# Kernel optimization log

Measured on AMD Instinct MI355X. Metric: run time of the kernel, lower is better.

Reference implementation:

```python
import jax, jax.numpy as jnp
import numpy as np


def setup_inputs() -> dict:
    key = jax.random.key(0)
    k1, k2 = jax.random.split(key)
    B, L, V, D = 8, 2048, 1024, 1024
    hidden_states = jax.random.normal(k1, (B, L, D), dtype=jnp.float32)
    visual_hidden_state = jax.random.normal(k2, (B, V, D), dtype=jnp.float32)
    return {"hidden_states": hidden_states, "visual_hidden_state": visual_hidden_state}


def reference(hidden_states, visual_hidden_state):
    # fusion_scores = H @ V^T  (no scaling, no masking)
    scores = jnp.einsum("bld,bvd->blv", hidden_states, visual_hidden_state)
    probs = jax.nn.softmax(scores, axis=-1)
    # fusion_output = probs @ V
    return jnp.einsum("blv,bvd->bld", probs, visual_hidden_state)
```

## Files before the change

### kernel.cpp

```cpp
#include <hip/hip_runtime.h>


typedef _Float16 half8_t __attribute__((ext_vector_type(8)));
typedef _Float16 half4_t __attribute__((ext_vector_type(4)));
typedef __fp16   fp16x2  __attribute__((ext_vector_type(2)));
typedef float    f32x4   __attribute__((ext_vector_type(4)));

#define B_ 8
#define L_ 2048
#define V_ 1024
#define D_ 1024

__device__ __forceinline__ half8_t cvt8(f32x4 a, f32x4 b) {
  union { half8_t h; fp16x2 p[4]; } u;
  u.p[0] = __builtin_amdgcn_cvt_pkrtz(a[0], a[1]);
  u.p[1] = __builtin_amdgcn_cvt_pkrtz(a[2], a[3]);
  u.p[2] = __builtin_amdgcn_cvt_pkrtz(b[0], b[1]);
  u.p[3] = __builtin_amdgcn_cvt_pkrtz(b[2], b[3]);
  return u.h;
}
__device__ __forceinline__ half4_t cvt4(f32x4 a) {
  union { half4_t h; fp16x2 p[2]; } u;
  u.p[0] = __builtin_amdgcn_cvt_pkrtz(a[0], a[1]);
  u.p[1] = __builtin_amdgcn_cvt_pkrtz(a[2], a[3]);
  return u.h;
}

__device__ __forceinline__ void gload_lds16(const _Float16* g, _Float16* l) {
  __builtin_amdgcn_global_load_lds(
      (const __attribute__((address_space(1))) unsigned int*)(g),
      (__attribute__((address_space(3))) unsigned int*)(l), 16, 0, 0);
}

__global__ __launch_bounds__(256) void p0_hconv(const float* __restrict__ H,
                                                _Float16* __restrict__ Hh) {
  const size_t i = ((size_t)blockIdx.x * 256 + threadIdx.x) * 8;
  f32x4 a = *(const f32x4*)(H + i);
  f32x4 b = *(const f32x4*)(H + i + 4);
  *(half8_t*)(Hh + i) = cvt8(a, b);
}

__global__ __launch_bounds__(256) void p1_vconv(const float* __restrict__ V,
                                                _Float16* __restrict__ Vh,
                                                _Float16* __restrict__ VTh) {
  const int b  = blockIdx.z;
  const int d0 = blockIdx.x * 64;
  const int v0 = blockIdx.y * 64;
  const float* Vb = V + (size_t)b * V_ * D_;
  __shared__ __align__(16) _Float16 Lt[64 * 80];
  const int t   = threadIdx.x;
  const int dc4 = (t & 15) * 4;
  #pragma unroll
  for (int it = 0; it < 4; ++it) {
    const int vr = (t >> 4) + it * 16;
    f32x4 x = *(const f32x4*)(Vb + (size_t)(v0 + vr) * D_ + d0 + dc4);
    half4_t h = cvt4(x);
    *(half4_t*)(Vh + (size_t)b * V_ * D_ + (size_t)(v0 + vr) * D_ + d0 + dc4) = h;
    #pragma unroll
    for (int j = 0; j < 4; ++j) Lt[(dc4 + j) * 80 + vr] = h[j];
  }
  __syncthreads();
  #pragma unroll
  for (int it = 0; it < 2; ++it) {
    const int dr = (t >> 3) + it * 32;
    const int vc = (t & 7) * 8;
    half8_t y = *(const half8_t*)&Lt[dr * 80 + vc];
    *(half8_t*)(VTh + (size_t)b * D_ * V_ + (size_t)(d0 + dr) * V_ + v0 + vc) = y;
  }
}

#define PH_BAR() asm volatile("s_barrier" ::: "memory")

__global__ __launch_bounds__(512, 2) void gemm256(
    const _Float16* __restrict__ A, const _Float16* __restrict__ B,
    float* __restrict__ C) {
  int lin = blockIdx.x;
  lin = (lin & 7) * 32 + (lin >> 3);
  const int bz = lin >> 5;
  const int my = (lin >> 2) & 7;
  const int nx = lin & 3;
  const int m0 = my * 256, n0 = nx * 256;

  const _Float16* Ap = A + (size_t)bz * (2048 * 1024) + (size_t)m0 * 1024;
  const _Float16* Bp = B + (size_t)bz * (1024 * 1024) + (size_t)n0 * 1024;
  float*          Cp = C + (size_t)bz * (2048 * 1024);

  __shared__ __align__(16) _Float16 As[2][16384];
  __shared__ __align__(16) _Float16 Bs[2][16384];

  const int t    = threadIdx.x;
  const int lane = t & 63;
  const int wid  = t >> 6;
  const int wm   = wid >> 2;
  const int wn   = wid & 3;
  const int fr   = lane & 15;
  const int fk   = lane >> 4;

  f32x4 acc[8][4];
  {
    f32x4 z = {0.f, 0.f, 0.f, 0.f};
    #pragma unroll
    for (int i = 0; i < 8; ++i)
      #pragma unroll
      for (int j = 0; j < 4; ++j) acc[i][j] = z;
  }

  #define STG(PTR, ARR, BUFL, H, KTT)                                          \
    {                                                                          \
      _Pragma("unroll")                                                        \
      for (int i_ = 0; i_ < 2; ++i_) {                                         \
        const int c_ = i_ * 512 + t;                                           \
        const int kg_ = c_ >> 7, r_ = c_ & 127;                                \
        gload_lds16(PTR + (size_t)((H) * 128 + r_) * 1024 + (KTT) * 64 + kg_ * 8, \
                    &ARR[BUFL][(kg_ * 256 + (H) * 128 + r_) * 8]);             \
      }                                                                        \
    }

  #define LDA(BUFL, mt_, ks_) \
    (*(const half8_t*)&As[BUFL][(((ks_) * 4 + fk) * 256 + wm * 128 + (mt_) * 16 + fr) * 8])
  #define LDB(BUFL, nt_, ks_) \
    (*(const half8_t*)&Bs[BUFL][(((ks_) * 4 + fk) * 256 + wn * 64 + (nt_) * 16 + fr) * 8])

  #define MFMA16(AF, BF, MOFF, NOFF)                                           \
    __builtin_amdgcn_s_setprio(1);                                             \
    _Pragma("unroll")                                                          \
    for (int ks = 0; ks < 2; ++ks)                                             \
      _Pragma("unroll")                                                        \
      for (int nt = 0; nt < 2; ++nt)                                           \
        _Pragma("unroll")                                                      \
        for (int mt = 0; mt < 4; ++mt)                                         \
          acc[(MOFF) + mt][(NOFF) + nt] =                                      \
              __builtin_amdgcn_mfma_f32_16x16x32_f16(                          \
                  AF[mt][ks], BF[nt][ks], acc[(MOFF) + mt][(NOFF) + nt], 0, 0, 0); \
    __builtin_amdgcn_s_setprio(0);

  #define TILE(KT, BUFL)                                                       \
    {                                                                          \
      half8_t a[4][2], b0[2][2], b1[2][2];                                     \
                         \
      _Pragma("unroll")                                                        \
      for (int ks = 0; ks < 2; ++ks) {                                         \
        _Pragma("unroll")                                                      \
        for (int mt = 0; mt < 4; ++mt) a[mt][ks] = LDA(BUFL, mt, ks);          \
        _Pragma("unroll")                                                      \
        for (int nt = 0; nt < 2; ++nt) b0[nt][ks] = LDB(BUFL, nt, ks);         \
      }                                                                        \
      PH_BAR();                                                                \
      MFMA16(a, b0, 0, 0)                                                      \
      PH_BAR();                                                                \
                   \
      _Pragma("unroll")                                                        \
      for (int ks = 0; ks < 2; ++ks)                                           \
        _Pragma("unroll")                                                      \
        for (int nt = 0; nt < 2; ++nt) b1[nt][ks] = LDB(BUFL, 2 + nt, ks);     \
      if ((KT) < 14) { STG(Bp, Bs, BUFL, 0, (KT) + 2) }                        \
      PH_BAR();                                                                \
      MFMA16(a, b1, 0, 2)                                                      \
      PH_BAR();                                                                \
                   \
      _Pragma("unroll")                                                        \
      for (int ks = 0; ks < 2; ++ks)                                           \
        _Pragma("unroll")                                                      \
        for (int mt = 0; mt < 4; ++mt) a[mt][ks] = LDA(BUFL, 4 + mt, ks);      \
      if ((KT) < 14) { STG(Bp, Bs, BUFL, 1, (KT) + 2) }                        \
      PH_BAR();                                                                \
      MFMA16(a, b1, 4, 2)                                                      \
      PH_BAR();                                                                \
                \
      if ((KT) < 14) { STG(Ap, As, BUFL, 0, (KT) + 2) STG(Ap, As, BUFL, 1, (KT) + 2) } \
      PH_BAR();                                                                \
      MFMA16(a, b0, 4, 0)                                                      \
      if ((KT) <= 13) {                                                        \
        asm volatile("s_waitcnt vmcnt(8)" ::: "memory");                       \
      } else if ((KT) == 14) {                                                 \
        asm volatile("s_waitcnt vmcnt(0)" ::: "memory");                       \
      }                                                                        \
      PH_BAR();                                                                \
    }

  STG(Bp, Bs, 0, 0, 0) STG(Ap, As, 0, 0, 0) STG(Bp, Bs, 0, 1, 0) STG(Ap, As, 0, 1, 0)
  STG(Bp, Bs, 1, 0, 1) STG(Ap, As, 1, 0, 1) STG(Bp, Bs, 1, 1, 1) STG(Ap, As, 1, 1, 1)
  asm volatile("s_waitcnt vmcnt(8)" ::: "memory");
  PH_BAR();

  #pragma unroll 1
  for (int ktp = 0; ktp < 8; ++ktp) {
    TILE(2 * ktp, 0)
    TILE(2 * ktp + 1, 1)
  }
  #undef TILE
  #undef STG
  #undef LDA
  #undef LDB
  #undef MFMA16

  const int rq = (lane >> 4) * 4;
  const int cb = n0 + wn * 64 + (lane & 15);
  const int rb = m0 + wm * 128 + rq;
  #pragma unroll
  for (int mt = 0; mt < 8; ++mt)
    #pragma unroll
    for (int nt = 0; nt < 4; ++nt) {
      #pragma unroll
      for (int r = 0; r < 4; ++r)
        Cp[(size_t)(rb + mt * 16 + r) * 1024 + cb + nt * 16] = acc[mt][nt][r];
    }
}

__global__ __launch_bounds__(256) void k2_softmax(const float* __restrict__ S,
                                                  _Float16* __restrict__ P) {
  const int t    = threadIdx.x;
  const int lane = t & 63;
  const int row  = blockIdx.x * 4 + (t >> 6);
  const float* Sr = S + (size_t)row * V_;

  f32x4 s[4];
  #pragma unroll
  for (int j = 0; j < 4; ++j) s[j] = *(const f32x4*)(Sr + (lane + 64 * j) * 4);

  float m = -1e30f;
  #pragma unroll
  for (int j = 0; j < 4; ++j)
    m = fmaxf(m, fmaxf(fmaxf(s[j][0], s[j][1]), fmaxf(s[j][2], s[j][3])));
  #pragma unroll
  for (int off = 1; off < 64; off <<= 1) m = fmaxf(m, __shfl_xor(m, off, 64));

  float sum = 0.f;
  #pragma unroll
  for (int j = 0; j < 4; ++j) {
    s[j][0] = __expf(s[j][0] - m); s[j][1] = __expf(s[j][1] - m);
    s[j][2] = __expf(s[j][2] - m); s[j][3] = __expf(s[j][3] - m);
    sum += (s[j][0] + s[j][1]) + (s[j][2] + s[j][3]);
  }
  #pragma unroll
  for (int off = 1; off < 64; off <<= 1) sum += __shfl_xor(sum, off, 64);
  const float inv = 1.0f / sum;

  _Float16* Pr = P + (size_t)row * V_;
  #pragma unroll
  for (int j = 0; j < 4; ++j) {
    f32x4 e = {s[j][0] * inv, s[j][1] * inv, s[j][2] * inv, s[j][3] * inv};
    *(half4_t*)(Pr + (lane + 64 * j) * 4) = cvt4(e);
  }
}

__global__ __launch_bounds__(256, 2) void k1_slow(
    const float* __restrict__ H, const float* __restrict__ Vv, float* __restrict__ S) {
  const int b  = blockIdx.z;
  const int m0 = blockIdx.y * 128;
  const int n0 = blockIdx.x * 128;
  const float* Hb = H  + (size_t)b * L_ * D_;
  const float* Vb = Vv + (size_t)b * V_ * D_;
  float*       Sb = S  + (size_t)b * L_ * V_;
  __shared__ __align__(16) _Float16 As[2][4096];
  __shared__ __align__(16) _Float16 Bs[2][4096];
  const int t = threadIdx.x, lane = t & 63, wm = (t >> 6) >> 1, wn = (t >> 6) & 1;
  f32x4 acc[4][4];
  { f32x4 z = {0,0,0,0};
    #pragma unroll
    for (int i = 0; i < 4; ++i)
      #pragma unroll
      for (int j = 0; j < 4; ++j) acc[i][j] = z; }
  const int skg = t & 3, sm = t >> 2;
  for (int kt = 0; kt < 32; ++kt) {
    const int kbase = kt * 32 + skg * 8, buf = kt & 1;
    #pragma unroll
    for (int h = 0; h < 2; ++h) {
      const int m = sm + h * 64;
      const float* sa = Hb + (size_t)(m0 + m) * D_ + kbase;
      const float* sb = Vb + (size_t)(n0 + m) * D_ + kbase;
      const int cell = skg * 128 + (m ^ (skg * 2));
      *(half8_t*)&As[buf][cell * 8] = cvt8(*(const f32x4*)sa, *(const f32x4*)(sa + 4));
      *(half8_t*)&Bs[buf][cell * 8] = cvt8(*(const f32x4*)sb, *(const f32x4*)(sb + 4));
    }
    __syncthreads();
    const int fkg = lane >> 4, fr = lane & 15;
    half8_t af[4];
    #pragma unroll
    for (int mt = 0; mt < 4; ++mt)
      af[mt] = *(const half8_t*)&As[buf][(fkg * 128 + ((wm * 64 + mt * 16 + fr) ^ (fkg * 2))) * 8];
    #pragma unroll
    for (int nt = 0; nt < 4; ++nt) {
      half8_t bf = *(const half8_t*)&Bs[buf][(fkg * 128 + ((wn * 64 + nt * 16 + fr) ^ (fkg * 2))) * 8];
      #pragma unroll
      for (int mt = 0; mt < 4; ++mt)
        acc[mt][nt] = __builtin_amdgcn_mfma_f32_16x16x32_f16(af[mt], bf, acc[mt][nt], 0, 0, 0);
    }
  }
  const int rq = (lane >> 4) * 4;
  #pragma unroll
  for (int mt = 0; mt < 4; ++mt)
    #pragma unroll
    for (int nt = 0; nt < 4; ++nt) {
      const int col = n0 + wn * 64 + nt * 16 + (lane & 15);
      const int rb  = m0 + wm * 64 + mt * 16 + rq;
      #pragma unroll
      for (int r = 0; r < 4; ++r) Sb[(size_t)(rb + r) * V_ + col] = acc[mt][nt][r];
    }
}

__global__ __launch_bounds__(256) void k2_slow(float* __restrict__ S) {
  const int row = blockIdx.x;
  float* Sr = S + (size_t)row * V_;
  const int t = threadIdx.x;
  f32x4 s = ((const f32x4*)Sr)[t];
  float m = fmaxf(fmaxf(s[0], s[1]), fmaxf(s[2], s[3]));
  #pragma unroll
  for (int off = 1; off < 64; off <<= 1) m = fmaxf(m, __shfl_xor(m, off, 64));
  __shared__ float redm[4];
  __shared__ float reds[4];
  const int w = t >> 6;
  if ((t & 63) == 0) redm[w] = m;
  __syncthreads();
  m = fmaxf(fmaxf(redm[0], redm[1]), fmaxf(redm[2], redm[3]));
  const float e0 = __expf(s[0] - m), e1 = __expf(s[1] - m);
  const float e2 = __expf(s[2] - m), e3 = __expf(s[3] - m);
  float sum = (e0 + e1) + (e2 + e3);
  #pragma unroll
  for (int off = 1; off < 64; off <<= 1) sum += __shfl_xor(sum, off, 64);
  if ((t & 63) == 0) reds[w] = sum;
  __syncthreads();
  const float inv = 1.0f / ((reds[0] + reds[1]) + (reds[2] + reds[3]));
  half4_t p;
  p[0] = (_Float16)(e0 * inv); p[1] = (_Float16)(e1 * inv);
  p[2] = (_Float16)(e2 * inv); p[3] = (_Float16)(e3 * inv);
  *(half4_t*)((_Float16*)Sr + 4 * t) = p;
}

__global__ __launch_bounds__(512, 2) void k3_slow(
    const float* __restrict__ Vv, float* __restrict__ O) {
  const int b = blockIdx.y, r0 = blockIdx.x * 64;
  const float* Vb = Vv + (size_t)b * V_ * D_;
  float*       Ob = O  + (size_t)b * L_ * D_;
  const _Float16* Pb = (const _Float16*)Ob;
  __shared__ __align__(16) _Float16 Bs[32768];
  const int t = threadIdx.x, lane = t & 63, w = t >> 6;
  f32x4 acc[4][8];
  { f32x4 z = {0,0,0,0};
    #pragma unroll
    for (int i = 0; i < 4; ++i)
      #pragma unroll
      for (int j = 0; j < 8; ++j) acc[i][j] = z; }
  for (int kt = 0; kt < 32; ++kt) {
    const int v0 = kt * 32;
    #pragma unroll
    for (int i = 0; i < 8; ++i) {
      const int c = t + i * 512, kg = c >> 10, d = c & 1023;
      const float* src = Vb + (size_t)(v0 + kg * 8) * D_ + d;
      f32x4 x0, x1;
      x0[0] = src[0*D_]; x0[1] = src[1*D_]; x0[2] = src[2*D_]; x0[3] = src[3*D_];
      x1[0] = src[4*D_]; x1[1] = src[5*D_]; x1[2] = src[6*D_]; x1[3] = src[7*D_];
      *(half8_t*)&Bs[(kg * 1024 + d) * 8] = cvt8(x0, x1);
    }
    __syncthreads();
    const int fkg = lane >> 4, fr = lane & 15;
    half8_t af[4];
    #pragma unroll
    for (int mt = 0; mt < 4; ++mt)
      af[mt] = *(const half8_t*)(Pb + (size_t)(r0 + mt * 16 + fr) * 2048 + v0 + fkg * 8);
    #pragma unroll
    for (int nt = 0; nt < 8; ++nt) {
      half8_t bf = *(const half8_t*)&Bs[(fkg * 1024 + w * 128 + nt * 16 + fr) * 8];
      #pragma unroll
      for (int mt = 0; mt < 4; ++mt)
        acc[mt][nt] = __builtin_amdgcn_mfma_f32_16x16x32_f16(af[mt], bf, acc[mt][nt], 0, 0, 0);
    }
    __syncthreads();
  }
  const int rq = (lane >> 4) * 4;
  #pragma unroll
  for (int mt = 0; mt < 4; ++mt)
    #pragma unroll
    for (int nt = 0; nt < 8; ++nt) {
      const int col = w * 128 + nt * 16 + (lane & 15);
      const int rb  = r0 + mt * 16 + rq;
      #pragma unroll
      for (int r = 0; r < 4; ++r) Ob[(size_t)(rb + r) * D_ + col] = acc[mt][nt][r];
    }
}

extern "C" void kernel_launch(void* const* d_in, const int* in_sizes, int n_in,
                              void* d_out, int out_size, void* d_ws, size_t ws_size,
                              hipStream_t stream) {
  (void)in_sizes; (void)n_in; (void)out_size;
  const float* H  = (const float*)d_in[0];
  const float* Vv = (const float*)d_in[1];
  float* O = (float*)d_out;

  const size_t need = (size_t)64 * 1024 * 1024;
  if (ws_size >= need && d_ws != nullptr) {
    _Float16* Hh  = (_Float16*)d_ws;
    _Float16* Vh  = Hh + (size_t)B_ * L_ * D_;
    _Float16* VTh = Vh + (size_t)B_ * V_ * D_;
    _Float16* P   = Hh;

    p0_hconv<<<dim3((B_ * L_ * D_) / (256 * 8)), 256, 0, stream>>>(H, Hh);
    p1_vconv<<<dim3(D_ / 64, V_ / 64, B_), 256, 0, stream>>>(Vv, Vh, VTh);
    gemm256<<<dim3(256), 512, 0, stream>>>(Hh, Vh, O);
    k2_softmax<<<dim3(B_ * L_ / 4), 256, 0, stream>>>(O, P);
    gemm256<<<dim3(256), 512, 0, stream>>>(P, VTh, O);
  } else {
    k1_slow<<<dim3(V_ / 128, L_ / 128, B_), 256, 0, stream>>>(H, Vv, O);
    k2_slow<<<dim3(B_ * L_), 256, 0, stream>>>(O);
    k3_slow<<<dim3(L_ / 64, B_), 512, 0, stream>>>(Vv, O);
  }
}
```

Before: 255.0 us.

## Merge conversion kernels and simplify GEMM pipeline to one-tile-ahead prefetch

Fuses the H and V fp16 conversion kernels into one launch that dispatches on block index, removing one kernel launch. The GEMM main loop drops the fine-grained staggered prefetch, the per-phase barriers and the setprio hints. Instead it issues the whole next tile's global-to-LDS loads at the start of each tile and waits on vmcnt(0) plus a single barrier at the end. This trades deeper, finer-grained overlap for fewer barriers, so memory latency may be less hidden and MFMA issue priority is lost.

```diff
diff --git a/kernel.cpp b/kernel.cpp
--- a/kernel.cpp
+++ b/kernel.cpp
@@ -32,23 +32,25 @@
       (__attribute__((address_space(3))) unsigned int*)(l), 16, 0, 0);
 }
 
-__global__ __launch_bounds__(256) void p0_hconv(const float* __restrict__ H,
-                                                _Float16* __restrict__ Hh) {
-  const size_t i = ((size_t)blockIdx.x * 256 + threadIdx.x) * 8;
-  f32x4 a = *(const f32x4*)(H + i);
-  f32x4 b = *(const f32x4*)(H + i + 4);
-  *(half8_t*)(Hh + i) = cvt8(a, b);
-}
-
-__global__ __launch_bounds__(256) void p1_vconv(const float* __restrict__ V,
+__global__ __launch_bounds__(256) void p01_conv(const float* __restrict__ H,
+                                                _Float16* __restrict__ Hh,
+                                                const float* __restrict__ V,
                                                 _Float16* __restrict__ Vh,
                                                 _Float16* __restrict__ VTh) {
-  const int b  = blockIdx.z;
-  const int d0 = blockIdx.x * 64;
-  const int v0 = blockIdx.y * 64;
+  const int t = threadIdx.x;
+  if (blockIdx.x < 8192) {
+    const size_t i = ((size_t)blockIdx.x * 256 + t) * 8;
+    f32x4 a = *(const f32x4*)(H + i);
+    f32x4 b = *(const f32x4*)(H + i + 4);
+    *(half8_t*)(Hh + i) = cvt8(a, b);
+    return;
+  }
+  const int lin = blockIdx.x - 8192;
+  const int b   = lin >> 8;
+  const int d0  = (lin & 15) * 64;
+  const int v0  = ((lin >> 4) & 15) * 64;
   const float* Vb = V + (size_t)b * V_ * D_;
   __shared__ __align__(16) _Float16 Lt[64 * 80];
-  const int t   = threadIdx.x;
   const int dc4 = (t & 15) * 4;
   #pragma unroll
   for (int it = 0; it < 4; ++it) {
@@ -68,8 +70,6 @@
     *(half8_t*)(VTh + (size_t)b * D_ * V_ + (size_t)(d0 + dr) * V_ + v0 + vc) = y;
   }
 }
-
-#define PH_BAR() asm volatile("s_barrier" ::: "memory")
 
 __global__ __launch_bounds__(512, 2) void gemm256(
     const _Float16* __restrict__ A, const _Float16* __restrict__ B,
@@ -115,6 +115,9 @@
                     &ARR[BUFL][(kg_ * 256 + (H) * 128 + r_) * 8]);             \
       }                                                                        \
     }
+  #define STGTILE(BUFL, KTT) \
+    STG(Bp, Bs, BUFL, 0, KTT) STG(Ap, As, BUFL, 0, KTT) \
+    STG(Bp, Bs, BUFL, 1, KTT) STG(Ap, As, BUFL, 1, KTT)
 
   #define LDA(BUFL, mt_, ks_) \
     (*(const half8_t*)&As[BUFL][(((ks_) * 4 + fk) * 256 + wm * 128 + (mt_) * 16 + fr) * 8])
@@ -122,7 +125,6 @@
     (*(const half8_t*)&Bs[BUFL][(((ks_) * 4 + fk) * 256 + wn * 64 + (nt_) * 16 + fr) * 8])
 
   #define MFMA16(AF, BF, MOFF, NOFF)                                           \
-    __builtin_amdgcn_s_setprio(1);                                             \
     _Pragma("unroll")                                                          \
     for (int ks = 0; ks < 2; ++ks)                                             \
       _Pragma("unroll")                                                        \
@@ -131,13 +133,13 @@
         for (int mt = 0; mt < 4; ++mt)                                         \
           acc[(MOFF) + mt][(NOFF) + nt] =                                      \
               __builtin_amdgcn_mfma_f32_16x16x32_f16(                          \
-                  AF[mt][ks], BF[nt][ks], acc[(MOFF) + mt][(NOFF) + nt], 0, 0, 0); \
-    __builtin_amdgcn_s_setprio(0);
-
-  #define TILE(KT, BUFL)                                                       \
+                  AF[mt][ks], BF[nt][ks], acc[(MOFF) + mt][(NOFF) + nt], 0, 0, 0);
+
+  #define TILE(KT, BUFL, OTH)                                                  \
     {                                                                          \
+      if ((KT) < 15) { STGTILE(OTH, (KT) + 1) }                                \
+      __builtin_amdgcn_sched_barrier(0);            \
       half8_t a[4][2], b0[2][2], b1[2][2];                                     \
-                         \
       _Pragma("unroll")                                                        \
       for (int ks = 0; ks < 2; ++ks) {                                         \
         _Pragma("unroll")                                                      \
@@ -145,65 +147,50 @@
         _Pragma("unroll")                                                      \
         for (int nt = 0; nt < 2; ++nt) b0[nt][ks] = LDB(BUFL, nt, ks);         \
       }                                                                        \
-      PH_BAR();                                                                \
       MFMA16(a, b0, 0, 0)                                                      \
-      PH_BAR();                                                                \
-                   \
       _Pragma("unroll")                                                        \
       for (int ks = 0; ks < 2; ++ks)                                           \
         _Pragma("unroll")                                                      \
         for (int nt = 0; nt < 2; ++nt) b1[nt][ks] = LDB(BUFL, 2 + nt, ks);     \
-      if ((KT) < 14) { STG(Bp, Bs, BUFL, 0, (KT) + 2) }                        \
-      PH_BAR();                                                                \
       MFMA16(a, b1, 0, 2)                                                      \
-      PH_BAR();                                                                \
-                   \
       _Pragma("unroll")                                                        \
       for (int ks = 0; ks < 2; ++ks)                                           \
         _Pragma("unroll")                                                      \
         for (int mt = 0; mt < 4; ++mt) a[mt][ks] = LDA(BUFL, 4 + mt, ks);      \
-      if ((KT) < 14) { STG(Bp, Bs, BUFL, 1, (KT) + 2) }                        \
-      PH_BAR();                                                                \
       MFMA16(a, b1, 4, 2)                                                      \
-      PH_BAR();                                                                \
-                \
-      if ((KT) < 14) { STG(Ap, As, BUFL, 0, (KT) + 2) STG(Ap, As, BUFL, 1, (KT) + 2) } \
-      PH_BAR();                                                                \
       MFMA16(a, b0, 4, 0)                                                      \
-      if ((KT) <= 13) {                                                        \
-        asm volatile("s_waitcnt vmcnt(8)" ::: "memory");                       \
-      } else if ((KT) == 14) {                                                 \
+      if ((KT) < 15) {                                                         \
         asm volatile("s_waitcnt vmcnt(0)" ::: "memory");                       \
+        __builtin_amdgcn_s_barrier();                                          \
       }                                                                        \
-      PH_BAR();                                                                \
-    }
-
-  STG(Bp, Bs, 0, 0, 0) STG(Ap, As, 0, 0, 0) STG(Bp, Bs, 0, 1, 0) STG(Ap, As, 0, 1, 0)
-  STG(Bp, Bs, 1, 0, 1) STG(Ap, As, 1, 0, 1) STG(Bp, Bs, 1, 1, 1) STG(Ap, As, 1, 1, 1)
-  asm volatile("s_waitcnt vmcnt(8)" ::: "memory");
-  PH_BAR();
+    }
+
+  STGTILE(0, 0)
+  asm volatile("s_waitcnt vmcnt(0)" ::: "memory");
+  __builtin_amdgcn_s_barrier();
 
   #pragma unroll 1
-  for (int ktp = 0; ktp < 8; ++ktp) {
-    TILE(2 * ktp, 0)
-    TILE(2 * ktp + 1, 1)
+  for (int tp = 0; tp < 8; ++tp) {
+    TILE(2 * tp, 0, 1)
+    TILE(2 * tp + 1, 1, 0)
   }
   #undef TILE
+  #undef STGTILE
   #undef STG
   #undef LDA
   #undef LDB
   #undef MFMA16
 
   const int rq = (lane >> 4) * 4;
-  const int cb = n0 + wn * 64 + (lane & 15);
-  const int rb = m0 + wm * 128 + rq;
   #pragma unroll
   for (int mt = 0; mt < 8; ++mt)
     #pragma unroll
     for (int nt = 0; nt < 4; ++nt) {
+      const int col   = n0 + wn * 64 + nt * 16 + (lane & 15);
+      const int rbase = m0 + wm * 128 + mt * 16 + rq;
       #pragma unroll
       for (int r = 0; r < 4; ++r)
-        Cp[(size_t)(rb + mt * 16 + r) * 1024 + cb + nt * 16] = acc[mt][nt][r];
+        Cp[(size_t)(rbase + r) * 1024 + col] = acc[mt][nt][r];
     }
 }
 
@@ -394,8 +381,7 @@
     _Float16* VTh = Vh + (size_t)B_ * V_ * D_;
     _Float16* P   = Hh;
 
-    p0_hconv<<<dim3((B_ * L_ * D_) / (256 * 8)), 256, 0, stream>>>(H, Hh);
-    p1_vconv<<<dim3(D_ / 64, V_ / 64, B_), 256, 0, stream>>>(Vv, Vh, VTh);
+    p01_conv<<<dim3(8192 + 2048), 256, 0, stream>>>(H, Hh, Vv, Vh, VTh);
     gemm256<<<dim3(256), 512, 0, stream>>>(Hh, Vh, O);
     k2_softmax<<<dim3(B_ * L_ / 4), 256, 0, stream>>>(O, P);
     gemm256<<<dim3(256), 512, 0, stream>>>(P, VTh, O);
```

New measurement: 265.5 us. 1.04x slower.
